# Kernel tuning notes

Hardware: AMD Instinct MI355X
Metric: run time of the kernel (lower is better)

Reference implementation:

```python
import jax, jax.numpy as jnp
import numpy as np

K = 5  # kernel_size


def _unfold(x, k):
    """Torch F.unfold equivalent: [B,C,H,W] -> [B,C,k*k,H,W].
    Patch index is row-major over the kxk window (dy*k+dx), matching
    F.unfold's channel-major / window-row-major layout after view(B,C,k*k,H,W)."""
    p = k // 2
    B, C, H, W = x.shape
    xp = jnp.pad(x, ((0, 0), (0, 0), (p, p), (p, p)))
    patches = [xp[:, :, dy:dy + H, dx:dx + W] for dy in range(k) for dx in range(k)]
    return jnp.stack(patches, axis=2)


def _conv2d(x, w, b, pad):
    y = jax.lax.conv_general_dilated(
        x, w, window_strides=(1, 1), padding=[(pad, pad), (pad, pad)],
        dimension_numbers=("NCHW", "OIHW", "NCHW"))
    return y + b[None, :, None, None]


def setup_inputs() -> dict:
    key = jax.random.key(0)
    k0, k1, k2 = jax.random.split(key, 3)
    B, H, W = 2, 1024, 1024
    flow = jax.random.normal(k0, (B, 2, H, W), jnp.float32)
    # kernel_gen params: Conv2d(3,32,3,pad=1) -> ReLU -> Conv2d(32,50,1)
    w1 = jax.random.normal(k1, (32, 3, 3, 3), jnp.float32) * 0.1
    b1 = jnp.zeros((32,), jnp.float32)
    w2 = jax.random.normal(k2, (K * K * 2, 32, 1, 1), jnp.float32) * 0.1
    b2 = jnp.zeros((K * K * 2,), jnp.float32)
    return {"flow": flow, "w1": w1, "b1": b1, "w2": w2, "b2": b2}


def reference(flow, w1, b1, w2, b2):
    B, _, H, W = flow.shape
    patches = _unfold(flow, K)                       # [B,2,25,H,W]
    # torch .var(dim=2) defaults to unbiased (ddof=1)
    var = jnp.var(patches, axis=2, ddof=1)           # [B,2,H,W]
    consistency = jnp.exp(-jnp.sqrt(jnp.sum(var * var, axis=1, keepdims=True)))  # [B,1,H,W]
    guidance = jnp.concatenate([flow, consistency], axis=1)  # [B,3,H,W]
    h = jax.nn.relu(_conv2d(guidance, w1, b1, pad=1))        # [B,32,H,W]
    kernels = _conv2d(h, w2, b2, pad=0).reshape(B, 2, K * K, H, W)
    refined = jnp.sum(kernels * patches, axis=2)             # [B,2,H,W]
    return refined
```

## Files before the change

kernel.cpp:

```cpp
#include <hip/hip_runtime.h>
#include <math.h>

#define KSZ 5
#define TSX 16
#define TSY 32
#define HALO 3
#define FWX 22
#define FH  38
#define PITCH 23
#define SF_C (FH*PITCH)
#define SC_BASE (2*SF_C)
#define SMF_TOT (SC_BASE + 34*PITCH)

typedef __attribute__((ext_vector_type(8))) short short8_t;
typedef __attribute__((ext_vector_type(4))) float float4_t;
typedef __attribute__((ext_vector_type(2))) unsigned int uint2_t;

static __device__ __forceinline__ unsigned short f2bf(float f) {
    union { float f; unsigned int u; } v; v.f = f;
    return (unsigned short)((v.u + 0x7FFFu + ((v.u >> 16) & 1u)) >> 16);
}
static __device__ __forceinline__ unsigned int pk2t(float a, float b) {
    union { float f; unsigned int u; } ua, ub; ua.f = a; ub.f = b;
    return __builtin_amdgcn_perm(ub.u, ua.u, 0x07060302u);
}

static __device__ __forceinline__ void slot_decode(int n, int& c, int& sel, int& idx, bool& valid) {
    int g4c = (n >> 2) & 3;
    c = g4c >> 1; sel = g4c & 1;
    idx = ((n >> 4) << 2) + (n & 3);
    valid = sel ? (idx < 10) : (idx < 15);
}

static __device__ __forceinline__ int kperm(int s) {
    int sg = s >> 3, sj = s & 7;
    if (sg < 3) return sg*9 + sj;
    if (sj == 1) return 8;
    if (sj == 2) return 17;
    if (sj == 4) return 26;
    return -1;
}

__global__ __launch_bounds__(256)
void pack_kernel(const float* __restrict__ w1, const float* __restrict__ b1,
                 const float* __restrict__ w2, const float* __restrict__ b2,
                 unsigned short* __restrict__ wp, float* __restrict__ bp)
{
    const int tid = threadIdx.x;
    for (int i = tid; i < 6*64*8; i += 256) {
        int f = i >> 9, l = (i >> 3) & 63, j = i & 7;
        int m = l & 15, s = ((l >> 4) << 3) + j;
        float v;
        if (f < 2) {
            int k = kperm(s);
            v = (k >= 0) ? w1[(f*16 + m)*27 + k] : 0.f;
        } else {
            int n = (f - 2)*16 + m;
            int c, sel, idx; bool valid;
            slot_decode(n, c, sel, idx, valid);
            v = valid ? w2[(c*25 + sel*15 + idx)*32 + s] : 0.f;
        }
        wp[i] = f2bf(v);
    }
    for (int i = tid; i < 6*64*4; i += 256) {
        int f = i >> 8, l = (i >> 2) & 63, r = i & 3, g4 = l >> 4;
        float v;
        if (f < 2) v = b1[f*16 + g4*4 + r];
        else {
            int n = (f - 2)*16 + g4*4 + r;
            int c, sel, idx; bool valid;
            slot_decode(n, c, sel, idx, valid);
            v = valid ? b2[c*25 + sel*15 + idx] : 0.f;
        }
        bp[i] = v;
    }
}

__global__ __launch_bounds__(256)
void refine_kernel(const float* __restrict__ flow,
                   const unsigned short* __restrict__ wp,
                   const float* __restrict__ bp,
                   float* __restrict__ out, int H, int W)
{
    __shared__ float smf[SMF_TOT];
    __shared__ __align__(16) char dyn[10960];

    const int tid = threadIdx.x;
    const int x0 = blockIdx.x * TSX;
    const int y0 = blockIdx.y * TSY;
    const int b  = blockIdx.z;

    const int lane = tid & 63;
    const int wave = tid >> 6;
    const int col  = lane & 15;
    const int g4   = lane >> 4;
    const int key  = col >> 2;

    short8_t w1A[2], w2A[4];
    float4_t cb1[2], cb2[4];
    #pragma unroll
    for (int nt = 0; nt < 2; ++nt) {
        w1A[nt] = *(const short8_t*)&wp[(nt*64 + lane)*8];
        cb1[nt] = *(const float4_t*)&bp[(nt*64 + lane)*4];
    }
    #pragma unroll
    for (int nt = 0; nt < 4; ++nt) {
        w2A[nt] = *(const short8_t*)&wp[((2+nt)*64 + lane)*8];
        cb2[nt] = *(const float4_t*)&bp[((2+nt)*64 + lane)*4];
    }

    {
        const float* srcb = flow + (size_t)(b*2) * H * W;
        if (x0 >= HALO && x0 + TSX + HALO <= W && y0 >= HALO && y0 + TSY + HALO <= H) {
            const float* s = srcb + (size_t)(y0 - HALO) * W + (x0 - HALO);
            for (int i = tid; i < 2*FH*FWX; i += 256) {
                int c = 0, r = i;
                if (r >= FH*FWX) { c = 1; r -= FH*FWX; }
                int ly = r / FWX, lx = r - ly*FWX;
                smf[c*SF_C + ly*PITCH + lx] = s[(size_t)c*H*W + ly*W + lx];
            }
        } else {
            for (int i = tid; i < 2*FH*FWX; i += 256) {
                int c = 0, r = i;
                if (r >= FH*FWX) { c = 1; r -= FH*FWX; }
                int ly = r / FWX, lx = r - ly*FWX;
                int gy = y0 - HALO + ly, gx = x0 - HALO + lx;
                float v = 0.f;
                if (gy >= 0 && gy < H && gx >= 0 && gx < W)
                    v = srcb[(size_t)c*H*W + (size_t)gy*W + gx];
                smf[c*SF_C + ly*PITCH + lx] = v;
            }
        }
    }
    __syncthreads();

    {
        float4_t* rs = (float4_t*)dyn;
        for (int i = tid; i < FH*9; i += 256) {
            int y = i / 9, xp = (i - y*9) * 2;
            const float* r0 = &smf[y*PITCH + xp];
            const float* r1 = &smf[SF_C + y*PITCH + xp];
            float a0=r0[0], a1=r0[1], a2=r0[2], a3=r0[3], a4=r0[4], a5=r0[5];
            float c0=r1[0], c1=r1[1], c2=r1[2], c3=r1[3], c4=r1[4], c5=r1[5];
            float sA = ((a0+a1)+(a2+a3))+a4;
            float qA = fmaf(a4,a4, fmaf(a3,a3, fmaf(a2,a2, fmaf(a1,a1, a0*a0))));
            float sB = ((c0+c1)+(c2+c3))+c4;
            float qB = fmaf(c4,c4, fmaf(c3,c3, fmaf(c2,c2, fmaf(c1,c1, c0*c0))));
            float sA1 = sA + a5 - a0;
            float qA1 = fmaf(-a0, a0, fmaf(a5, a5, qA));
            float sB1 = sB + c5 - c0;
            float qB1 = fmaf(-c0, c0, fmaf(c5, c5, qB));
            rs[y*18 + xp]     = (float4_t){sA,  qA,  sB,  qB };
            rs[y*18 + xp + 1] = (float4_t){sA1, qA1, sB1, qB1};
        }
    }
    __syncthreads();

    for (int i = tid; i < 34*18; i += 256) {
        int py = i / 18, px = i - py*18;
        int gy = y0 - 1 + py, gx = x0 - 1 + px;
        float cons = 0.f;
        if (gy >= 0 && gy < H && gx >= 0 && gx < W) {
            const float4_t* rp = (const float4_t*)dyn + py*18 + px;
            float4_t acc = rp[0];
            #pragma unroll
            for (int dy = 1; dy < KSZ; ++dy) acc += rp[dy*18];
            float v0 = (acc.y - acc.x*acc.x*(1.f/25.f)) * (1.f/24.f);
            float v1 = (acc.w - acc.z*acc.z*(1.f/25.f)) * (1.f/24.f);
            cons = __expf(-sqrtf(v0*v0 + v1*v1));
        }
        smf[SC_BASE + py*PITCH + px] = cons;
    }
    __syncthreads();

    unsigned short* hb = (unsigned short*)dyn;

    int gb0, gb1, gb2, gb3;
    {
        int ty0 = wave*8;
        int p0 = 0*SF_C + (ty0 + 2)*PITCH + (col + 2);
        int p1 = 1*SF_C + (ty0 + 2)*PITCH + (col + 2);
        int p2 = SC_BASE + ty0*PITCH + col;
        if (g4 == 0)      { gb0 = gb1 = gb2 = gb3 = p0; }
        else if (g4 == 1) { gb0 = gb1 = gb2 = gb3 = p1; }
        else if (g4 == 2) { gb0 = gb1 = gb2 = gb3 = p2; }
        else { gb0 = p0 + 47; gb1 = p1 + 46; gb2 = p2 + 24; gb3 = p0; }
    }

    const int sel = g4 & 1, pc = g4 >> 1;
    int pb = pc*SF_C + sel*(3*PITCH) + PITCH + 1 + col + (wave*8)*PITCH;
    float pv[15];
    #pragma unroll
    for (int i = 0; i < 15; ++i) pv[i] = smf[pb + (i/5)*PITCH + (i%5)];

    const int hrow = (wave*16 + col) * 64;
    const int hw0 = hrow + (((0*2 + pc) ^ key) << 4) + (sel << 3);
    const int hw1 = hrow + (((1*2 + pc) ^ key) << 4) + (sel << 3);
    const int hro = hrow + ((g4 ^ key) << 4);

    #pragma unroll
    for (int mt = 0; mt < 8; ++mt) {
        const int ty = wave*8 + mt;

        float ga = smf[gb0 + 0],  gbv = smf[gb0 + 1];
        float gc = smf[gb1 + 2],  gd  = smf[gb1 + 23];
        float ge = smf[gb2 + 24], gf  = smf[gb2 + 25];
        float gg = smf[gb3 + 46], gh  = smf[gb3 + 47];
        union { unsigned int u[4]; short8_t s; } gu;
        gu.u[0] = pk2t(ga, gbv); gu.u[1] = pk2t(gc, gd);
        gu.u[2] = pk2t(ge, gf);  gu.u[3] = pk2t(gg, gh);
        short8_t gB = gu.s;
        gb0 += PITCH; gb1 += PITCH; gb2 += PITCH; gb3 += PITCH;

        float4_t h0 = __builtin_amdgcn_mfma_f32_16x16x32_bf16(w1A[0], gB, cb1[0], 0, 0, 0);
        float4_t h1 = __builtin_amdgcn_mfma_f32_16x16x32_bf16(w1A[1], gB, cb1[1], 0, 0, 0);

        {
            uint2_t d0, d1;
            d0.x = pk2t(fmaxf(h0[0],0.f), fmaxf(h0[1],0.f));
            d0.y = pk2t(fmaxf(h0[2],0.f), fmaxf(h0[3],0.f));
            d1.x = pk2t(fmaxf(h1[0],0.f), fmaxf(h1[1],0.f));
            d1.y = pk2t(fmaxf(h1[2],0.f), fmaxf(h1[3],0.f));
            *(uint2_t*)((char*)hb + hw0) = d0;
            *(uint2_t*)((char*)hb + hw1) = d1;
        }
        short8_t hf = *(const short8_t*)((char*)hb + hro);

        float4_t ka[4];
        #pragma unroll
        for (int nt = 0; nt < 4; ++nt)
            ka[nt] = __builtin_amdgcn_mfma_f32_16x16x32_bf16(w2A[nt], hf, cb2[nt], 0, 0, 0);

        float s = 0.f;
        #pragma unroll
        for (int i = 0; i < 15; ++i)
            s = fmaf(ka[i >> 2][i & 3], pv[i], s);

        if (mt < 7) {
            #pragma unroll
            for (int i = 0; i < 10; ++i) pv[i] = pv[i + 5];
            pb += PITCH;
            #pragma unroll
            for (int i = 10; i < 15; ++i) pv[i] = smf[pb + (i/5)*PITCH + (i%5)];
        }

        s += __shfl_xor(s, 16);

        if (sel == 0) {
            int y = y0 + ty, x = x0 + col;
            out[((size_t)(b*2 + pc) * H + y) * W + x] = s;
        }
    }
}

extern "C" void kernel_launch(void* const* d_in, const int* in_sizes, int n_in,
                              void* d_out, int out_size, void* d_ws, size_t ws_size,
                              hipStream_t stream) {
    const float* flow = (const float*)d_in[0];
    const float* w1   = (const float*)d_in[1];
    const float* b1   = (const float*)d_in[2];
    const float* w2   = (const float*)d_in[3];
    const float* b2   = (const float*)d_in[4];
    float* out = (float*)d_out;

    unsigned short* wp = (unsigned short*)d_ws;
    float* bp = (float*)((char*)d_ws + 8192);

    const int H = 1024, W = 1024;
    const int B = in_sizes[0] / (2 * H * W);

    pack_kernel<<<1, 256, 0, stream>>>(w1, b1, w2, b2, wp, bp);
    dim3 grid(W / TSX, H / TSY, B);
    refine_kernel<<<grid, dim3(256), 0, stream>>>(flow, wp, bp, out, H, W);
}
```

Baseline: 118.7 us.

## Feed MFMA hidden activations directly from registers and double tile height

The first MFMA's output is now packed straight into the B operand of the second MFMA. To make this possible, the K-dimension ordering of the packed w2 weights is permuted to match the accumulator layout, which removes the LDS write/read round-trip for the hidden layer. The tile height also doubles from 32 to 64 rows, so each wave processes 16 rows and the halo overhead per output shrinks. In exchange the kernel uses more shared memory, has a longer unrolled loop that raises register pressure, and launches fewer blocks.

```diff
diff --git a/kernel.cpp b/kernel.cpp
--- a/kernel.cpp
+++ b/kernel.cpp
@@ -3,18 +3,18 @@
 
 #define KSZ 5
 #define TSX 16
-#define TSY 32
+#define TSY 64
 #define HALO 3
 #define FWX 22
-#define FH  38
+#define FH  70
+#define SCH 66
 #define PITCH 23
 #define SF_C (FH*PITCH)
 #define SC_BASE (2*SF_C)
-#define SMF_TOT (SC_BASE + 34*PITCH)
+#define SMF_TOT (SC_BASE + SCH*PITCH)
 
 typedef __attribute__((ext_vector_type(8))) short short8_t;
 typedef __attribute__((ext_vector_type(4))) float float4_t;
-typedef __attribute__((ext_vector_type(2))) unsigned int uint2_t;
 
 static __device__ __forceinline__ unsigned short f2bf(float f) {
     union { float f; unsigned int u; } v; v.f = f;
@@ -39,6 +39,11 @@
     if (sj == 2) return 17;
     if (sj == 4) return 26;
     return -1;
+}
+
+static __device__ __forceinline__ int kperm2(int s) {
+    int g = s >> 3, j = s & 7;
+    return (j < 4) ? (g*4 + j) : (16 + g*4 + (j - 4));
 }
 
 __global__ __launch_bounds__(256)
@@ -58,7 +63,7 @@
             int n = (f - 2)*16 + m;
             int c, sel, idx; bool valid;
             slot_decode(n, c, sel, idx, valid);
-            v = valid ? w2[(c*25 + sel*15 + idx)*32 + s] : 0.f;
+            v = valid ? w2[(c*25 + sel*15 + idx)*32 + kperm2(s)] : 0.f;
         }
         wp[i] = f2bf(v);
     }
@@ -83,7 +88,7 @@
                    float* __restrict__ out, int H, int W)
 {
     __shared__ float smf[SMF_TOT];
-    __shared__ __align__(16) char dyn[10960];
+    __shared__ __align__(16) float4_t rs[FH*18];
 
     const int tid = threadIdx.x;
     const int x0 = blockIdx.x * TSX;
@@ -94,7 +99,6 @@
     const int wave = tid >> 6;
     const int col  = lane & 15;
     const int g4   = lane >> 4;
-    const int key  = col >> 2;
 
     short8_t w1A[2], w2A[4];
     float4_t cb1[2], cb2[4];
@@ -134,34 +138,31 @@
     }
     __syncthreads();
 
-    {
-        float4_t* rs = (float4_t*)dyn;
-        for (int i = tid; i < FH*9; i += 256) {
-            int y = i / 9, xp = (i - y*9) * 2;
-            const float* r0 = &smf[y*PITCH + xp];
-            const float* r1 = &smf[SF_C + y*PITCH + xp];
-            float a0=r0[0], a1=r0[1], a2=r0[2], a3=r0[3], a4=r0[4], a5=r0[5];
-            float c0=r1[0], c1=r1[1], c2=r1[2], c3=r1[3], c4=r1[4], c5=r1[5];
-            float sA = ((a0+a1)+(a2+a3))+a4;
-            float qA = fmaf(a4,a4, fmaf(a3,a3, fmaf(a2,a2, fmaf(a1,a1, a0*a0))));
-            float sB = ((c0+c1)+(c2+c3))+c4;
-            float qB = fmaf(c4,c4, fmaf(c3,c3, fmaf(c2,c2, fmaf(c1,c1, c0*c0))));
-            float sA1 = sA + a5 - a0;
-            float qA1 = fmaf(-a0, a0, fmaf(a5, a5, qA));
-            float sB1 = sB + c5 - c0;
-            float qB1 = fmaf(-c0, c0, fmaf(c5, c5, qB));
-            rs[y*18 + xp]     = (float4_t){sA,  qA,  sB,  qB };
-            rs[y*18 + xp + 1] = (float4_t){sA1, qA1, sB1, qB1};
-        }
+    for (int i = tid; i < FH*9; i += 256) {
+        int y = i / 9, xp = (i - y*9) * 2;
+        const float* r0 = &smf[y*PITCH + xp];
+        const float* r1 = &smf[SF_C + y*PITCH + xp];
+        float a0=r0[0], a1=r0[1], a2=r0[2], a3=r0[3], a4=r0[4], a5=r0[5];
+        float c0=r1[0], c1=r1[1], c2=r1[2], c3=r1[3], c4=r1[4], c5=r1[5];
+        float sA = ((a0+a1)+(a2+a3))+a4;
+        float qA = fmaf(a4,a4, fmaf(a3,a3, fmaf(a2,a2, fmaf(a1,a1, a0*a0))));
+        float sB = ((c0+c1)+(c2+c3))+c4;
+        float qB = fmaf(c4,c4, fmaf(c3,c3, fmaf(c2,c2, fmaf(c1,c1, c0*c0))));
+        float sA1 = sA + a5 - a0;
+        float qA1 = fmaf(-a0, a0, fmaf(a5, a5, qA));
+        float sB1 = sB + c5 - c0;
+        float qB1 = fmaf(-c0, c0, fmaf(c5, c5, qB));
+        rs[y*18 + xp]     = (float4_t){sA,  qA,  sB,  qB };
+        rs[y*18 + xp + 1] = (float4_t){sA1, qA1, sB1, qB1};
     }
     __syncthreads();
 
-    for (int i = tid; i < 34*18; i += 256) {
+    for (int i = tid; i < SCH*18; i += 256) {
         int py = i / 18, px = i - py*18;
         int gy = y0 - 1 + py, gx = x0 - 1 + px;
         float cons = 0.f;
         if (gy >= 0 && gy < H && gx >= 0 && gx < W) {
-            const float4_t* rp = (const float4_t*)dyn + py*18 + px;
+            const float4_t* rp = rs + py*18 + px;
             float4_t acc = rp[0];
             #pragma unroll
             for (int dy = 1; dy < KSZ; ++dy) acc += rp[dy*18];
@@ -173,11 +174,9 @@
     }
     __syncthreads();
 
-    unsigned short* hb = (unsigned short*)dyn;
-
     int gb0, gb1, gb2, gb3;
     {
-        int ty0 = wave*8;
+        int ty0 = wave*16;
         int p0 = 0*SF_C + (ty0 + 2)*PITCH + (col + 2);
         int p1 = 1*SF_C + (ty0 + 2)*PITCH + (col + 2);
         int p2 = SC_BASE + ty0*PITCH + col;
@@ -188,19 +187,14 @@
     }
 
     const int sel = g4 & 1, pc = g4 >> 1;
-    int pb = pc*SF_C + sel*(3*PITCH) + PITCH + 1 + col + (wave*8)*PITCH;
+    int pb = pc*SF_C + sel*(3*PITCH) + PITCH + 1 + col + (wave*16)*PITCH;
     float pv[15];
     #pragma unroll
     for (int i = 0; i < 15; ++i) pv[i] = smf[pb + (i/5)*PITCH + (i%5)];
 
-    const int hrow = (wave*16 + col) * 64;
-    const int hw0 = hrow + (((0*2 + pc) ^ key) << 4) + (sel << 3);
-    const int hw1 = hrow + (((1*2 + pc) ^ key) << 4) + (sel << 3);
-    const int hro = hrow + ((g4 ^ key) << 4);
-
-    #pragma unroll
-    for (int mt = 0; mt < 8; ++mt) {
-        const int ty = wave*8 + mt;
+    #pragma unroll
+    for (int mt = 0; mt < 16; ++mt) {
+        const int ty = wave*16 + mt;
 
         float ga = smf[gb0 + 0],  gbv = smf[gb0 + 1];
         float gc = smf[gb1 + 2],  gd  = smf[gb1 + 23];
@@ -215,16 +209,12 @@
         float4_t h0 = __builtin_amdgcn_mfma_f32_16x16x32_bf16(w1A[0], gB, cb1[0], 0, 0, 0);
         float4_t h1 = __builtin_amdgcn_mfma_f32_16x16x32_bf16(w1A[1], gB, cb1[1], 0, 0, 0);
 
-        {
-            uint2_t d0, d1;
-            d0.x = pk2t(fmaxf(h0[0],0.f), fmaxf(h0[1],0.f));
-            d0.y = pk2t(fmaxf(h0[2],0.f), fmaxf(h0[3],0.f));
-            d1.x = pk2t(fmaxf(h1[0],0.f), fmaxf(h1[1],0.f));
-            d1.y = pk2t(fmaxf(h1[2],0.f), fmaxf(h1[3],0.f));
-            *(uint2_t*)((char*)hb + hw0) = d0;
-            *(uint2_t*)((char*)hb + hw1) = d1;
-        }
-        short8_t hf = *(const short8_t*)((char*)hb + hro);
+        union { unsigned int u[4]; short8_t s; } hu;
+        hu.u[0] = pk2t(fmaxf(h0[0],0.f), fmaxf(h0[1],0.f));
+        hu.u[1] = pk2t(fmaxf(h0[2],0.f), fmaxf(h0[3],0.f));
+        hu.u[2] = pk2t(fmaxf(h1[0],0.f), fmaxf(h1[1],0.f));
+        hu.u[3] = pk2t(fmaxf(h1[2],0.f), fmaxf(h1[3],0.f));
+        short8_t hf = hu.s;
 
         float4_t ka[4];
         #pragma unroll
@@ -236,7 +226,7 @@
         for (int i = 0; i < 15; ++i)
             s = fmaf(ka[i >> 2][i & 3], pv[i], s);
 
-        if (mt < 7) {
+        if (mt < 15) {
             #pragma unroll
             for (int i = 0; i < 10; ++i) pv[i] = pv[i + 5];
             pb += PITCH;
```

Result: faster. 115.6 us (-2.7%).
